# Kernel optimization log

Hardware: AMD Instinct MI355X
Metric: run time of the kernel (lower is better)

The kernel has to match this reference:

```python
import itertools
import jax, jax.numpy as jnp
import numpy as np

H, W = 512, 512
B, G, F, C = 2, 4, 9, 3
N = H * W


def _morton(pos):
    # pos: [N,3] int; interleave bits as in MortonFromPosition
    pos = np.asarray(pos, dtype=np.int32)
    code = np.zeros(len(pos), dtype=np.int64)
    coeff = np.asarray([4, 2, 1], dtype=np.int64)
    for b in range(21):
        code |= ((pos & (1 << b)) << (2 * b)) @ coeff
    return code


def _build_graph(h, w):
    xindex, yindex = np.meshgrid(np.arange(w), np.arange(h))
    xy = np.stack([yindex, xindex], axis=2).reshape(-1, 2)
    z = np.zeros((len(xy), 1), dtype=np.int64)
    hc = _morton(np.concatenate([xy, z], axis=1))
    order = np.argsort(hc)
    xy = xy[order]
    hc = hc[order]
    order_inv = np.zeros(len(xy), dtype=np.int32)
    order_inv[order] = np.arange(len(xy))
    deltas = np.array(list(itertools.product([-1, 0, 1], [-1, 0, 1])), dtype=np.int32)
    T = len(deltas)
    node_i = np.repeat(np.arange(len(xy), dtype=np.int32), T)
    loc_j = (xy[:, None, :] + deltas[None, :, :]).reshape(-1, 2)
    zc = np.zeros((len(loc_j), 1), dtype=np.int64)
    hj = _morton(np.concatenate([loc_j, zc], axis=1))
    pos = np.clip(np.searchsorted(hc, hj), 0, len(hc) - 1)
    valid = (hc[pos] == hj) & (loc_j[:, 0] >= 0) & (loc_j[:, 0] < h) \
            & (loc_j[:, 1] >= 0) & (loc_j[:, 1] < w)
    edges = np.stack([node_i[valid], pos[valid].astype(np.int32)], axis=1)
    return edges, order.astype(np.int32), order_inv


def setup_inputs() -> dict:
    key = jax.random.key(0)
    k1, k2, k3 = jax.random.split(key, 3)
    edges_np, order_np, order_inv_np = _build_graph(H, W)
    M_DIAG_INIT = 0.4
    multiM = jnp.eye(F, dtype=jnp.float32)[None, :, :] * M_DIAG_INIT
    multiM = jnp.tile(multiM, (G, 1, 1))
    return {
        "img_features": jax.random.normal(k1, (B, G, F, H, W), dtype=jnp.float32),
        "signals2d": jax.random.normal(k2, (B, G, C, H, W), dtype=jnp.float32),
        "multiM": multiM + 0.01 * jax.random.normal(k3, (G, F, F), dtype=jnp.float32),
        "edges": jnp.asarray(edges_np, dtype=jnp.int32),
        "order": jnp.asarray(order_np, dtype=jnp.int32),
        "order_inverse": jnp.asarray(order_inv_np, dtype=jnp.int32),
    }


def reference(img_features, signals2d, multiM, edges, order, order_inverse):
    b, g, f, h, w = img_features.shape
    n = h * w
    # F.normalize over feature dim (eps=1e-12)
    norm = jnp.sqrt(jnp.sum(img_features * img_features, axis=2, keepdims=True))
    feats = img_features / jnp.maximum(norm, 1e-12)
    # signal2D_to_graph_signals: flatten + Morton reorder
    node_feats = feats.reshape(b, g, f, n)[..., order]          # [b,g,f,n]
    fM = jnp.einsum('bgcn,gcv->bgvn', node_feats, multiM)        # [b,g,f,n]
    nodeI = edges[:, 0]
    nodeJ = edges[:, 1]
    sim = jnp.sum(fM[..., nodeI] * fM[..., nodeJ], axis=2)       # [b,g,E]
    ew = jnp.exp(jnp.clip(sim, -10.0, 10.0))                     # [b,g,E]
    # degree = scatter-add of edge weights by source node (== one-hot buffer sum)
    deg = jnp.zeros((b, g, n), dtype=ew.dtype).at[:, :, nodeI].add(ew)
    dinv = 1.0 / jnp.sqrt(deg)
    ew_n = dinv[:, :, nodeI] * ew * dinv[:, :, nodeJ]            # [b,g,E]
    # op_L_norm on graph signals
    sig = signals2d.reshape(b, g, -1, n)[..., order]             # [b,g,c,n]
    se = sig[..., nodeJ] * ew_n[:, :, None, :]                   # [b,g,c,E]
    agg = jnp.zeros_like(sig).at[:, :, :, nodeI].add(se)
    out = sig - agg
    # graph_signals_to_signal2D
    out2d = out[..., order_inverse].reshape(b, g, -1, h, w)
    return out2d
```

## Files before the change

kernel.cpp:

```cpp
#include <hip/hip_runtime.h>
#include <hip/hip_fp16.h>

#define Hh 512
#define Ww 512
#define Bb 2
#define Gg 4
#define Ff 9
#define Cc 3
#define Nn (Hh*Ww)

#define TILE 32
#define RS 36
#define RSP 37
#define DS 34
#define DSP 35
#define NT 256

typedef float f32x2 __attribute__((ext_vector_type(2)));

struct Fm8 { unsigned a, b; float cf; };

__device__ __forceinline__ float dot8(const Fm8& p, const Fm8& q) {
    f32x2 p01 = __builtin_amdgcn_cvt_pk_f32_fp8(p.a, false);
    f32x2 p23 = __builtin_amdgcn_cvt_pk_f32_fp8(p.a, true);
    f32x2 p45 = __builtin_amdgcn_cvt_pk_f32_fp8(p.b, false);
    f32x2 p67 = __builtin_amdgcn_cvt_pk_f32_fp8(p.b, true);
    f32x2 q01 = __builtin_amdgcn_cvt_pk_f32_fp8(q.a, false);
    f32x2 q23 = __builtin_amdgcn_cvt_pk_f32_fp8(q.a, true);
    f32x2 q45 = __builtin_amdgcn_cvt_pk_f32_fp8(q.b, false);
    f32x2 q67 = __builtin_amdgcn_cvt_pk_f32_fp8(q.b, true);
    float s = p01[0] * q01[0];
    s = fmaf(p01[1], q01[1], s);
    s = fmaf(p23[0], q23[0], s);
    s = fmaf(p23[1], q23[1], s);
    s = fmaf(p45[0], q45[0], s);
    s = fmaf(p45[1], q45[1], s);
    s = fmaf(p67[0], q67[0], s);
    s = fmaf(p67[1], q67[1], s);
    s = fmaf(p.cf, q.cf, s);
    return s;
}

__device__ __forceinline__ float ew_of(float s) {
    s = fminf(fmaxf(s, -10.f), 10.f);
    return __expf(s);
}

__global__ void __launch_bounds__(NT, 6) fused_kernel(const float* __restrict__ img,
                                                      const float* __restrict__ M,
                                                      const float* __restrict__ sig,
                                                      float* __restrict__ out) {
    __shared__ uint2   fm8[RS * RSP];
    __shared__ __half  fmC[RS * RSP];
    __shared__ float   dv[DS * DSP];

    const int tid = threadIdx.x;
    const int bg   = blockIdx.x & 7;
    const int tile = blockIdx.x >> 3;
    const int g    = bg & (Gg - 1);
    const int by0  = (tile >> 4) * TILE;
    const int bx0  = (tile & 15) * TILE;
    const bool border = (by0 == 0) | (by0 == Hh - TILE) | (bx0 == 0) | (bx0 == Ww - TILE);

    const float* imgP = img + (size_t)bg * Ff * Nn;
    const float* sgp  = sig + (size_t)bg * Cc * Nn;
    const float* Mg   = M + g * Ff * Ff;

    auto LD = [&](int idx) -> Fm8 {
        Fm8 p;
        uint2 w = fm8[idx];
        p.a = w.x; p.b = w.y;
        p.cf = __half2float(fmC[idx]);
        return p;
    };

    for (int i = tid; i < RS * RS; i += NT) {
        unsigned r = (unsigned)i / RS, c = (unsigned)i - r * RS;
        int gy = by0 - 2 + (int)r, gx = bx0 - 2 + (int)c;
        float m[Ff];
        if ((unsigned)gy < Hh && (unsigned)gx < Ww) {
            const float* src = imgP + gy * Ww + gx;
            float v[Ff]; float ss = 0.f;
#pragma unroll
            for (int f = 0; f < Ff; ++f) { v[f] = src[f * Nn]; ss += v[f] * v[f]; }
            float inv = 1.0f / fmaxf(sqrtf(ss), 1e-12f);
#pragma unroll
            for (int f = 0; f < Ff; ++f) v[f] *= inv;
#pragma unroll
            for (int vv = 0; vv < Ff; ++vv) {
                float acc = 0.f;
#pragma unroll
                for (int cc = 0; cc < Ff; ++cc) acc = fmaf(v[cc], Mg[cc * Ff + vv], acc);
                m[vv] = acc;
            }
        } else {
#pragma unroll
            for (int f = 0; f < Ff; ++f) m[f] = 0.f;
        }
        int si = r * RSP + c;
        int A = __builtin_amdgcn_cvt_pk_fp8_f32(m[0], m[1], 0, false);
        A     = __builtin_amdgcn_cvt_pk_fp8_f32(m[2], m[3], A, true);
        int Bw = __builtin_amdgcn_cvt_pk_fp8_f32(m[4], m[5], 0, false);
        Bw     = __builtin_amdgcn_cvt_pk_fp8_f32(m[6], m[7], Bw, true);
        fm8[si] = make_uint2((unsigned)A, (unsigned)Bw);
        fmC[si] = __float2half_rn(m[8]);
    }
    __syncthreads();

    const int r2 = tid >> 4, c2 = tid & 15;
    const int gy0 = by0 + 2 * r2, gx0 = bx0 + 2 * c2;
    const int wb  = (2 * r2 + 1) * RSP + (2 * c2 + 1);

    Fm8 w0[4], w1[4], w2[4], w3[4];
#pragma unroll
    for (int ci = 0; ci < 4; ++ci) w0[ci] = LD(wb + ci);
#pragma unroll
    for (int ci = 0; ci < 4; ++ci) w1[ci] = LD(wb + RSP + ci);
#pragma unroll
    for (int ci = 0; ci < 4; ++ci) w2[ci] = LD(wb + 2 * RSP + ci);

    float e0[9], e1[9], e2[9], e3[9];
    e0[0] = ew_of(dot8(w1[1], w0[0])); e0[1] = ew_of(dot8(w1[1], w0[1])); e0[2] = ew_of(dot8(w1[1], w0[2]));
    e0[3] = ew_of(dot8(w1[1], w1[0])); e0[4] = ew_of(dot8(w1[1], w1[1])); e0[5] = ew_of(dot8(w1[1], w1[2]));
    e0[6] = ew_of(dot8(w1[1], w2[0])); e0[7] = ew_of(dot8(w1[1], w2[1])); e0[8] = ew_of(dot8(w1[1], w2[2]));
    e1[0] = ew_of(dot8(w1[2], w0[1])); e1[1] = ew_of(dot8(w1[2], w0[2])); e1[2] = ew_of(dot8(w1[2], w0[3]));
    e1[3] = e0[5];                     e1[4] = ew_of(dot8(w1[2], w1[2])); e1[5] = ew_of(dot8(w1[2], w1[3]));
    e1[6] = ew_of(dot8(w1[2], w2[1])); e1[7] = ew_of(dot8(w1[2], w2[2])); e1[8] = ew_of(dot8(w1[2], w2[3]));

#pragma unroll
    for (int ci = 0; ci < 4; ++ci) w3[ci] = LD(wb + 3 * RSP + ci);

    e2[0] = ew_of(dot8(w2[1], w1[0])); e2[1] = e0[7];                     e2[2] = e1[6];
    e2[3] = ew_of(dot8(w2[1], w2[0])); e2[4] = ew_of(dot8(w2[1], w2[1])); e2[5] = ew_of(dot8(w2[1], w2[2]));
    e2[6] = ew_of(dot8(w2[1], w3[0])); e2[7] = ew_of(dot8(w2[1], w3[1])); e2[8] = ew_of(dot8(w2[1], w3[2]));
    e3[0] = e0[8];                     e3[1] = e1[7];                     e3[2] = ew_of(dot8(w2[2], w1[3]));
    e3[3] = e2[5];                     e3[4] = ew_of(dot8(w2[2], w2[2])); e3[5] = ew_of(dot8(w2[2], w2[3]));
    e3[6] = ew_of(dot8(w2[2], w3[1])); e3[7] = ew_of(dot8(w2[2], w3[2])); e3[8] = ew_of(dot8(w2[2], w3[3]));

    if (border) {
#pragma unroll
        for (int j = 0; j < 9; ++j) {
            int dy = j / 3 - 1, dx = j % 3 - 1;
            if (!(((unsigned)(gy0 + dy)     < Hh) & ((unsigned)(gx0 + dx)     < Ww))) e0[j] = 0.f;
            if (!(((unsigned)(gy0 + dy)     < Hh) & ((unsigned)(gx0 + 1 + dx) < Ww))) e1[j] = 0.f;
            if (!(((unsigned)(gy0 + 1 + dy) < Hh) & ((unsigned)(gx0 + dx)     < Ww))) e2[j] = 0.f;
            if (!(((unsigned)(gy0 + 1 + dy) < Hh) & ((unsigned)(gx0 + 1 + dx) < Ww))) e3[j] = 0.f;
        }
    }

    float deg0 = 0.f, deg1 = 0.f, deg2 = 0.f, deg3 = 0.f;
#pragma unroll
    for (int j = 0; j < 9; ++j) { deg0 += e0[j]; deg1 += e1[j]; deg2 += e2[j]; deg3 += e3[j]; }
    {
        const int db = (2 * r2 + 1) * DSP + (2 * c2 + 1);
        dv[db]           = 1.0f / sqrtf(deg0);
        dv[db + 1]       = 1.0f / sqrtf(deg1);
        dv[db + DSP]     = 1.0f / sqrtf(deg2);
        dv[db + DSP + 1] = 1.0f / sqrtf(deg3);
    }

    if (tid < 132) {
        int r, c;
        if (tid < 34)       { r = 0;        c = tid;       }
        else if (tid < 68)  { r = 33;       c = tid - 34;  }
        else if (tid < 100) { r = tid - 67; c = 0;         }
        else                { r = tid - 99; c = 33;        }
        int gy = by0 - 1 + r, gx = bx0 - 1 + c;
        float d = 1.0f;
        if ((unsigned)gy < Hh && (unsigned)gx < Ww) {
            int fi = (r + 1) * RSP + (c + 1);
            Fm8 a = LD(fi);
            float deg = 0.f;
#pragma unroll
            for (int j = 0; j < 9; ++j) {
                int dy = j / 3 - 1, dx = j % 3 - 1;
                Fm8 q = LD(fi + dy * RSP + dx);
                float e = ew_of(dot8(a, q));
                bool valid = ((unsigned)(gy + dy) < Hh) & ((unsigned)(gx + dx) < Ww);
                deg += valid ? e : 0.f;
            }
            d = 1.0f / sqrtf(deg);
        }
        dv[r * DSP + c] = d;
    }
    __syncthreads();

    float dvf[16];
    {
        const int db = 2 * r2 * DSP + 2 * c2;
#pragma unroll
        for (int k = 0; k < 16; ++k)
            dvf[k] = dv[db + (k >> 2) * DSP + (k & 3)];
    }
    const float dp0 = dvf[5], dp1 = dvf[6], dp2 = dvf[9], dp3 = dvf[10];
#pragma unroll
    for (int j = 0; j < 9; ++j) {
        const int k0 = (j / 3) * 4 + (j % 3);
        e0[j] = dp0 * e0[j] * dvf[k0];
        e1[j] = dp1 * e1[j] * dvf[k0 + 1];
        e2[j] = dp2 * e2[j] * dvf[k0 + 4];
        e3[j] = dp3 * e3[j] * dvf[k0 + 5];
    }

    int ry[4], cx[4];
#pragma unroll
    for (int i = 0; i < 4; ++i) {
        ry[i] = min(max(gy0 - 1 + i, 0), Hh - 1) * Ww;
        cx[i] = min(max(gx0 - 1 + i, 0), Ww - 1);
    }

    float* o = out + (size_t)bg * Cc * Nn;
    const int p = gy0 * Ww + gx0;
#pragma unroll
    for (int ch = 0; ch < Cc; ++ch) {
        const float* sc = sgp + (size_t)ch * Nn;
        float s[16];
#pragma unroll
        for (int k = 0; k < 16; ++k) s[k] = sc[ry[k >> 2] + cx[k & 3]];
        float a0 = 0.f, a1 = 0.f, a2 = 0.f, a3 = 0.f;
#pragma unroll
        for (int j = 0; j < 9; ++j) {
            const int k0 = (j / 3) * 4 + (j % 3);
            a0 = fmaf(e0[j], s[k0],     a0);
            a1 = fmaf(e1[j], s[k0 + 1], a1);
            a2 = fmaf(e2[j], s[k0 + 4], a2);
            a3 = fmaf(e3[j], s[k0 + 5], a3);
        }
        float* oc = o + (size_t)ch * Nn;
        *(float2*)&oc[p]      = make_float2(s[5] - a0, s[6]  - a1);
        *(float2*)&oc[p + Ww] = make_float2(s[9] - a2, s[10] - a3);
    }
}

extern "C" void kernel_launch(void* const* d_in, const int* in_sizes, int n_in,
                              void* d_out, int out_size, void* d_ws, size_t ws_size,
                              hipStream_t stream) {
    const float* img = (const float*)d_in[0];
    const float* sig = (const float*)d_in[1];
    const float* M   = (const float*)d_in[2];
    float* out = (float*)d_out;

    fused_kernel<<<dim3(256 * Bb * Gg), NT, 0, stream>>>(img, M, sig, out);
}
```

Baseline: 38.62 us.

## Stage degree-scaled signals in fp16 shared memory and aggregate with packed half FMAs

```diff
diff --git a/kernel.cpp b/kernel.cpp
--- a/kernel.cpp
+++ b/kernel.cpp
@@ -13,7 +13,7 @@
 #define RS 36
 #define RSP 37
 #define DS 34
-#define DSP 35
+#define SGS 36
 #define NT 256
 
 typedef float f32x2 __attribute__((ext_vector_type(2)));
@@ -46,13 +46,14 @@
     return __expf(s);
 }
 
-__global__ void __launch_bounds__(NT, 6) fused_kernel(const float* __restrict__ img,
+__global__ void __launch_bounds__(NT, 7) fused_kernel(const float* __restrict__ img,
                                                       const float* __restrict__ M,
                                                       const float* __restrict__ sig,
                                                       float* __restrict__ out) {
     __shared__ uint2   fm8[RS * RSP];
     __shared__ __half  fmC[RS * RSP];
-    __shared__ float   dv[DS * DSP];
+    __shared__ __half2 sgA[DS * SGS];
+    __shared__ __half  sgB[DS * SGS];
 
     const int tid = threadIdx.x;
     const int bg   = blockIdx.x & 7;
@@ -74,6 +75,18 @@
         return p;
     };
 
+    for (int i = tid; i < DS * DS; i += NT) {
+        unsigned r = (unsigned)i / DS, c = (unsigned)i - r * DS;
+        int gy = by0 - 1 + (int)r, gx = bx0 - 1 + (int)c;
+        float v0 = 0.f, v1 = 0.f, v2 = 0.f;
+        if ((unsigned)gy < Hh && (unsigned)gx < Ww) {
+            int q = gy * Ww + gx;
+            v0 = sgp[q]; v1 = sgp[Nn + q]; v2 = sgp[2 * Nn + q];
+        }
+        sgA[r * SGS + c] = __floats2half2_rn(v0, v1);
+        sgB[r * SGS + c] = __float2half_rn(v2);
+    }
+
     for (int i = tid; i < RS * RS; i += NT) {
         unsigned r = (unsigned)i / RS, c = (unsigned)i - r * RS;
         int gy = by0 - 2 + (int)r, gx = bx0 - 2 + (int)c;
@@ -151,12 +164,28 @@
     float deg0 = 0.f, deg1 = 0.f, deg2 = 0.f, deg3 = 0.f;
 #pragma unroll
     for (int j = 0; j < 9; ++j) { deg0 += e0[j]; deg1 += e1[j]; deg2 += e2[j]; deg3 += e3[j]; }
+    const float dp0 = 1.0f / sqrtf(deg0);
+    const float dp1 = 1.0f / sqrtf(deg1);
+    const float dp2 = 1.0f / sqrtf(deg2);
+    const float dp3 = 1.0f / sqrtf(deg3);
+
+    __half2 ep01[9], ep23[9];
+#pragma unroll
+    for (int j = 0; j < 9; ++j) {
+        ep01[j] = __floats2half2_rn(e0[j], e1[j]);
+        ep23[j] = __floats2half2_rn(e2[j], e3[j]);
+    }
+
     {
-        const int db = (2 * r2 + 1) * DSP + (2 * c2 + 1);
-        dv[db]           = 1.0f / sqrtf(deg0);
-        dv[db + 1]       = 1.0f / sqrtf(deg1);
-        dv[db + DSP]     = 1.0f / sqrtf(deg2);
-        dv[db + DSP + 1] = 1.0f / sqrtf(deg3);
+        const int db = (2 * r2 + 1) * SGS + (2 * c2 + 1);
+        sgA[db]           = __hmul2(sgA[db],           __float2half2_rn(dp0));
+        sgB[db]           = __hmul(sgB[db],            __float2half_rn(dp0));
+        sgA[db + 1]       = __hmul2(sgA[db + 1],       __float2half2_rn(dp1));
+        sgB[db + 1]       = __hmul(sgB[db + 1],        __float2half_rn(dp1));
+        sgA[db + SGS]     = __hmul2(sgA[db + SGS],     __float2half2_rn(dp2));
+        sgB[db + SGS]     = __hmul(sgB[db + SGS],      __float2half_rn(dp2));
+        sgA[db + SGS + 1] = __hmul2(sgA[db + SGS + 1], __float2half2_rn(dp3));
+        sgB[db + SGS + 1] = __hmul(sgB[db + SGS + 1],  __float2half_rn(dp3));
     }
 
     if (tid < 132) {
@@ -181,54 +210,65 @@
             }
             d = 1.0f / sqrtf(deg);
         }
-        dv[r * DSP + c] = d;
+        int si = r * SGS + c;
+        sgA[si] = __hmul2(sgA[si], __float2half2_rn(d));
+        sgB[si] = __hmul(sgB[si],  __float2half_rn(d));
     }
     __syncthreads();
 
-    float dvf[16];
-    {
-        const int db = 2 * r2 * DSP + 2 * c2;
-#pragma unroll
-        for (int k = 0; k < 16; ++k)
-            dvf[k] = dv[db + (k >> 2) * DSP + (k & 3)];
-    }
-    const float dp0 = dvf[5], dp1 = dvf[6], dp2 = dvf[9], dp3 = dvf[10];
+    const int sb = 2 * r2 * SGS + 2 * c2;
+    __half2 sA[16];
+    __half2 sBa[4], sBb[4];
+#pragma unroll
+    for (int kr = 0; kr < 4; ++kr) {
+        int idx = sb + kr * SGS;
+        *(uint2*)&sA[4 * kr]     = *(const uint2*)&sgA[idx];
+        *(uint2*)&sA[4 * kr + 2] = *(const uint2*)&sgA[idx + 2];
+        sBa[kr] = *(const __half2*)&sgB[idx];
+        sBb[kr] = *(const __half2*)&sgB[idx + 2];
+    }
+
+    __half2 g0 = __floats2half2_rn(0.f, 0.f), g1 = g0, g2 = g0, g3 = g0;
+    __half2 h01 = g0, h23 = g0;
 #pragma unroll
     for (int j = 0; j < 9; ++j) {
-        const int k0 = (j / 3) * 4 + (j % 3);
-        e0[j] = dp0 * e0[j] * dvf[k0];
-        e1[j] = dp1 * e1[j] * dvf[k0 + 1];
-        e2[j] = dp2 * e2[j] * dvf[k0 + 4];
-        e3[j] = dp3 * e3[j] * dvf[k0 + 5];
-    }
-
-    int ry[4], cx[4];
-#pragma unroll
-    for (int i = 0; i < 4; ++i) {
-        ry[i] = min(max(gy0 - 1 + i, 0), Hh - 1) * Ww;
-        cx[i] = min(max(gx0 - 1 + i, 0), Ww - 1);
-    }
+        const int jr = j / 3, jc = j % 3;
+        const int k0 = jr * 4 + jc;
+        g0 = __hfma2(__half2half2(__low2half(ep01[j])),  sA[k0],     g0);
+        g1 = __hfma2(__half2half2(__high2half(ep01[j])), sA[k0 + 1], g1);
+        g2 = __hfma2(__half2half2(__low2half(ep23[j])),  sA[k0 + 4], g2);
+        g3 = __hfma2(__half2half2(__high2half(ep23[j])), sA[k0 + 5], g3);
+        __half2 bTop = (jc == 0) ? sBa[jr] :
+                       (jc == 2) ? sBb[jr] :
+                       __halves2half2(__high2half(sBa[jr]), __low2half(sBb[jr]));
+        __half2 bBot = (jc == 0) ? sBa[jr + 1] :
+                       (jc == 2) ? sBb[jr + 1] :
+                       __halves2half2(__high2half(sBa[jr + 1]), __low2half(sBb[jr + 1]));
+        h01 = __hfma2(ep01[j], bTop, h01);
+        h23 = __hfma2(ep23[j], bBot, h23);
+    }
+
+    const float a00 = dp0 * __low2float(g0),  a01 = dp0 * __high2float(g0),  a02 = dp0 * __low2float(h01);
+    const float a10 = dp1 * __low2float(g1),  a11 = dp1 * __high2float(g1),  a12 = dp1 * __high2float(h01);
+    const float a20 = dp2 * __low2float(g2),  a21 = dp2 * __high2float(g2),  a22 = dp2 * __low2float(h23);
+    const float a30 = dp3 * __low2float(g3),  a31 = dp3 * __high2float(g3),  a32 = dp3 * __high2float(h23);
 
     float* o = out + (size_t)bg * Cc * Nn;
     const int p = gy0 * Ww + gx0;
-#pragma unroll
-    for (int ch = 0; ch < Cc; ++ch) {
-        const float* sc = sgp + (size_t)ch * Nn;
-        float s[16];
-#pragma unroll
-        for (int k = 0; k < 16; ++k) s[k] = sc[ry[k >> 2] + cx[k & 3]];
-        float a0 = 0.f, a1 = 0.f, a2 = 0.f, a3 = 0.f;
-#pragma unroll
-        for (int j = 0; j < 9; ++j) {
-            const int k0 = (j / 3) * 4 + (j % 3);
-            a0 = fmaf(e0[j], s[k0],     a0);
-            a1 = fmaf(e1[j], s[k0 + 1], a1);
-            a2 = fmaf(e2[j], s[k0 + 4], a2);
-            a3 = fmaf(e3[j], s[k0 + 5], a3);
-        }
-        float* oc = o + (size_t)ch * Nn;
-        *(float2*)&oc[p]      = make_float2(s[5] - a0, s[6]  - a1);
-        *(float2*)&oc[p + Ww] = make_float2(s[9] - a2, s[10] - a3);
+    {
+        float2 s0 = *(const float2*)&sgp[p];
+        float2 s1 = *(const float2*)&sgp[Nn + p];
+        float2 s2 = *(const float2*)&sgp[2 * Nn + p];
+        *(float2*)&o[p]          = make_float2(s0.x - a00, s0.y - a10);
+        *(float2*)&o[Nn + p]     = make_float2(s1.x - a01, s1.y - a11);
+        *(float2*)&o[2 * Nn + p] = make_float2(s2.x - a02, s2.y - a12);
+        const int pb = p + Ww;
+        s0 = *(const float2*)&sgp[pb];
+        s1 = *(const float2*)&sgp[Nn + pb];
+        s2 = *(const float2*)&sgp[2 * Nn + pb];
+        *(float2*)&o[pb]          = make_float2(s0.x - a20, s0.y - a30);
+        *(float2*)&o[Nn + pb]     = make_float2(s1.x - a21, s1.y - a31);
+        *(float2*)&o[2 * Nn + pb] = make_float2(s2.x - a22, s2.y - a32);
     }
 }
 
```

Result: slower. 48.98 us (+26.8%).
